# Performance work log

Measured on AMD Instinct MI355X. Metric: run time of the kernel, lower is better.

## Reference

```python
import jax, jax.numpy as jnp
import numpy as np

TAU = 0.95
COEF = 0.5
LOG_CLAMP = -100.0  # torch BCELoss clamps log terms at -100


def setup_inputs() -> dict:
    key = jax.random.key(0)
    k1, k2, k3, k4, k5 = jax.random.split(key, 5)
    B, L = 4096, 2048
    eps = 1e-4
    # probabilities in (eps, 1-eps) so log / log1p are finite
    def prob(k, shape):
        return jax.random.uniform(k, shape, dtype=jnp.float32, minval=eps, maxval=1.0 - eps)
    truncation_output = prob(k1, (B, L, 1))
    view_1_output = prob(k2, (B, L, 1))
    view_2_output = prob(k3, (B, L, 1))
    view_3_output = prob(k4, (B, L, 1))
    labels = (jax.random.uniform(k5, (B, L)) < 0.1).astype(jnp.float32)
    return {
        "truncation_output": truncation_output,
        "view_1_output": view_1_output,
        "view_2_output": view_2_output,
        "view_3_output": view_3_output,
        "labels": labels,
    }


def _bce_div_batch(p, y):
    # nn.BCELoss() (mean reduction) then .div(batch_size)
    logp = jnp.maximum(jnp.log(p), LOG_CLAMP)
    log1mp = jnp.maximum(jnp.log1p(-p), LOG_CLAMP)
    bce = -jnp.mean(y * logp + (1.0 - y) * log1mp)
    return bce / p.shape[0]


def _f1_matrix(labels):
    # r[i, j] = F1(labels[i], cutoff=j+1), vectorized via cumsum
    B, L = labels.shape
    cum = jnp.cumsum(labels, axis=1)                       # rel@(j+1)
    k = jnp.arange(1, L + 1, dtype=labels.dtype)           # cutoff
    total = cum[:, -1:]                                    # total relevant per row
    # P = cum/k, R = cum/total -> F1 = 2*cum/(k+total); 0 when no hits
    return jnp.where(cum > 0, 2.0 * cum / (k + total), 0.0)


def reference(truncation_output, view_1_output, view_2_output, view_3_output, labels):
    B = truncation_output.shape[0]
    v1 = _bce_div_batch(view_1_output[..., 0], labels)
    v2 = _bce_div_batch(view_2_output[..., 0], labels)
    v3 = _bce_div_batch(view_3_output[..., 0], labels)

    r = _f1_matrix(labels)                                 # [B, L]
    q = jax.nn.softmax(r / TAU, axis=-1)                   # softmax over list dim
    log_out = jnp.log(truncation_output[..., 0] / TAU)
    trunc_loss = -jnp.sum(log_out * q) / B

    return COEF * trunc_loss + (1.0 - COEF) * (v1 + v2 + v3)
```

## Files before the change

### kernel.cpp

```cpp
#include <hip/hip_runtime.h>

#define B_DIM 4096
#define L_DIM 2048
#define TPB   256
#define EPT   8
#define TAU_INV 1.0526315789473684f

__global__ __launch_bounds__(TPB) void milecut_row_kernel(
    const float* __restrict__ trunc,
    const float* __restrict__ view1,
    const float* __restrict__ view2,
    const float* __restrict__ view3,
    const float* __restrict__ labels,
    float* __restrict__ partials)
{
    const int row = blockIdx.x;
    const int t   = threadIdx.x;
    const size_t rowOff = (size_t)row * L_DIM;

    __shared__ float sdata[TPB];

    const float4* y4 = (const float4*)(labels + rowOff) + t * 2;
    float4 ya = y4[0];
    float4 yb = y4[1];
    float y[EPT] = {ya.x, ya.y, ya.z, ya.w, yb.x, yb.y, yb.z, yb.w};

    float lsum = 0.f;
    #pragma unroll
    for (int k = 0; k < EPT; ++k) lsum += y[k];

    sdata[t] = lsum;
    __syncthreads();
    for (int off = 1; off < TPB; off <<= 1) {
        float v   = sdata[t];
        float add = (t >= off) ? sdata[t - off] : 0.f;
        __syncthreads();
        sdata[t] = v + add;
        __syncthreads();
    }
    float total = sdata[TPB - 1];
    float run   = (t > 0) ? sdata[t - 1] : 0.f;
    __syncthreads();

    float x[EPT];
    float m = 0.f;
    #pragma unroll
    for (int k = 0; k < EPT; ++k) {
        run += y[k];
        float denom = (float)(t * EPT + k + 1) + total;
        float r = (run > 0.f) ? (2.f * run) / denom : 0.f;
        x[k] = r * TAU_INV;
        m = fmaxf(m, x[k]);
    }

    sdata[t] = m;
    __syncthreads();
    for (int off = TPB / 2; off > 0; off >>= 1) {
        if (t < off) sdata[t] = fmaxf(sdata[t], sdata[t + off]);
        __syncthreads();
    }
    m = sdata[0];
    __syncthreads();

    float esum = 0.f;
    #pragma unroll
    for (int k = 0; k < EPT; ++k) { x[k] = __expf(x[k] - m); esum += x[k]; }

    sdata[t] = esum;
    __syncthreads();
    for (int off = TPB / 2; off > 0; off >>= 1) {
        if (t < off) sdata[t] += sdata[t + off];
        __syncthreads();
    }
    float s = sdata[0];
    __syncthreads();

    const float4* t4 = (const float4*)(trunc + rowOff) + t * 2;
    float4 ta = t4[0];
    float4 tb = t4[1];
    float tv[EPT] = {ta.x, ta.y, ta.z, ta.w, tb.x, tb.y, tb.z, tb.w};
    float wtr = 0.f;
    #pragma unroll
    for (int k = 0; k < EPT; ++k) wtr += __logf(tv[k] * TAU_INV) * x[k];

    float bce = 0.f;
    const float* views[3] = {view1, view2, view3};
    #pragma unroll
    for (int vi = 0; vi < 3; ++vi) {
        const float4* p4 = (const float4*)(views[vi] + rowOff) + t * 2;
        float4 pa = p4[0];
        float4 pb = p4[1];
        float pv[EPT] = {pa.x, pa.y, pa.z, pa.w, pb.x, pb.y, pb.z, pb.w};
        #pragma unroll
        for (int k = 0; k < EPT; ++k) {
            float sel = (y[k] > 0.5f) ? pv[k] : (1.0f - pv[k]);
            bce += fmaxf(__logf(sel), -100.0f);
        }
    }

    sdata[t] = wtr;
    __syncthreads();
    for (int off = TPB / 2; off > 0; off >>= 1) {
        if (t < off) sdata[t] += sdata[t + off];
        __syncthreads();
    }
    float wsum = sdata[0];
    __syncthreads();

    sdata[t] = bce;
    __syncthreads();
    for (int off = TPB / 2; off > 0; off >>= 1) {
        if (t < off) sdata[t] += sdata[t + off];
        __syncthreads();
    }

    if (t == 0) {
        partials[row]         = wsum / s;
        partials[B_DIM + row] = sdata[0];
    }
}

__global__ __launch_bounds__(TPB) void milecut_final_kernel(
    const float* __restrict__ partials, float* __restrict__ out)
{
    const int t = threadIdx.x;
    float st = 0.f, sb = 0.f;
    for (int i = t; i < B_DIM; i += TPB) {
        st += partials[i];
        sb += partials[B_DIM + i];
    }
    __shared__ float s1[TPB];
    __shared__ float s2[TPB];
    s1[t] = st; s2[t] = sb;
    __syncthreads();
    for (int off = TPB / 2; off > 0; off >>= 1) {
        if (t < off) { s1[t] += s1[t + off]; s2[t] += s2[t + off]; }
        __syncthreads();
    }
    if (t == 0) {
        double St = (double)s1[0];
        double Sb = (double)s2[0];
        double trunc_loss = -St / (double)B_DIM;
        double vsum = -Sb / ((double)B_DIM * (double)L_DIM * (double)B_DIM);
        out[0] = (float)(0.5 * trunc_loss + 0.5 * vsum);
    }
}

extern "C" void kernel_launch(void* const* d_in, const int* in_sizes, int n_in,
                              void* d_out, int out_size, void* d_ws, size_t ws_size,
                              hipStream_t stream) {
    const float* trunc  = (const float*)d_in[0];
    const float* v1     = (const float*)d_in[1];
    const float* v2     = (const float*)d_in[2];
    const float* v3     = (const float*)d_in[3];
    const float* labels = (const float*)d_in[4];

    float* partials = (float*)d_ws;

    milecut_row_kernel<<<B_DIM, TPB, 0, stream>>>(trunc, v1, v2, v3, labels, partials);
    milecut_final_kernel<<<1, TPB, 0, stream>>>(partials, (float*)d_out);
}
```

Measured before the change: 180.3 us.

## Replace shared-memory block reductions with wavefront shuffles and hoist all loads

Replaces the shared-memory Hillis-Steele scan and tree reductions, which use many __syncthreads, with wavefront shuffle scans and reductions that need only two block barriers. All five input rows are loaded up front so their memory latency overlaps. The softmax max-subtraction pass is dropped because the F1 values lie in [0,1], so exp without the shift stays bounded; this removes one reduction. The gain is fewer barriers and less LDS traffic, at the cost of higher register pressure from holding all inputs at once.

```diff
diff --git a/kernel.cpp b/kernel.cpp
--- a/kernel.cpp
+++ b/kernel.cpp
@@ -4,6 +4,7 @@
 #define L_DIM 2048
 #define TPB   256
 #define EPT   8
+#define NWAVE (TPB / 64)
 #define TAU_INV 1.0526315789473684f
 
 __global__ __launch_bounds__(TPB) void milecut_row_kernel(
@@ -14,109 +15,98 @@
     const float* __restrict__ labels,
     float* __restrict__ partials)
 {
-    const int row = blockIdx.x;
-    const int t   = threadIdx.x;
+    const int row  = blockIdx.x;
+    const int t    = threadIdx.x;
+    const int lane = t & 63;
+    const int wave = t >> 6;
     const size_t rowOff = (size_t)row * L_DIM;
 
-    __shared__ float sdata[TPB];
+    const float4* y4 = (const float4*)(labels + rowOff) + t * 2;
+    const float4* t4 = (const float4*)(trunc  + rowOff) + t * 2;
+    const float4* p1 = (const float4*)(view1  + rowOff) + t * 2;
+    const float4* p2 = (const float4*)(view2  + rowOff) + t * 2;
+    const float4* p3 = (const float4*)(view3  + rowOff) + t * 2;
+    float4 ya = y4[0], yb = y4[1];
+    float4 ta = t4[0], tb = t4[1];
+    float4 v1a = p1[0], v1b = p1[1];
+    float4 v2a = p2[0], v2b = p2[1];
+    float4 v3a = p3[0], v3b = p3[1];
 
-    const float4* y4 = (const float4*)(labels + rowOff) + t * 2;
-    float4 ya = y4[0];
-    float4 yb = y4[1];
-    float y[EPT] = {ya.x, ya.y, ya.z, ya.w, yb.x, yb.y, yb.z, yb.w};
+    float y[EPT]  = {ya.x, ya.y, ya.z, ya.w, yb.x, yb.y, yb.z, yb.w};
 
     float lsum = 0.f;
     #pragma unroll
     for (int k = 0; k < EPT; ++k) lsum += y[k];
 
-    sdata[t] = lsum;
+    float v = lsum;
+    #pragma unroll
+    for (int off = 1; off < 64; off <<= 1) {
+        float n = __shfl_up(v, off, 64);
+        if (lane >= off) v += n;
+    }
+    float waveTotal = __shfl(v, 63, 64);
+
+    __shared__ float wtot[NWAVE];
+    __shared__ float red[NWAVE][3];
+    if (lane == 63) wtot[wave] = waveTotal;
     __syncthreads();
-    for (int off = 1; off < TPB; off <<= 1) {
-        float v   = sdata[t];
-        float add = (t >= off) ? sdata[t - off] : 0.f;
-        __syncthreads();
-        sdata[t] = v + add;
-        __syncthreads();
+    float wavePrefix = 0.f, total = 0.f;
+    #pragma unroll
+    for (int w = 0; w < NWAVE; ++w) {
+        float wt = wtot[w];
+        if (w < wave) wavePrefix += wt;
+        total += wt;
     }
-    float total = sdata[TPB - 1];
-    float run   = (t > 0) ? sdata[t - 1] : 0.f;
-    __syncthreads();
+    float run = wavePrefix + (v - lsum);
 
     float x[EPT];
-    float m = 0.f;
+    float esum = 0.f;
     #pragma unroll
     for (int k = 0; k < EPT; ++k) {
         run += y[k];
         float denom = (float)(t * EPT + k + 1) + total;
         float r = (run > 0.f) ? (2.f * run) / denom : 0.f;
-        x[k] = r * TAU_INV;
-        m = fmaxf(m, x[k]);
+        x[k] = __expf(r * TAU_INV);
+        esum += x[k];
     }
 
-    sdata[t] = m;
-    __syncthreads();
-    for (int off = TPB / 2; off > 0; off >>= 1) {
-        if (t < off) sdata[t] = fmaxf(sdata[t], sdata[t + off]);
-        __syncthreads();
-    }
-    m = sdata[0];
-    __syncthreads();
-
-    float esum = 0.f;
-    #pragma unroll
-    for (int k = 0; k < EPT; ++k) { x[k] = __expf(x[k] - m); esum += x[k]; }
-
-    sdata[t] = esum;
-    __syncthreads();
-    for (int off = TPB / 2; off > 0; off >>= 1) {
-        if (t < off) sdata[t] += sdata[t + off];
-        __syncthreads();
-    }
-    float s = sdata[0];
-    __syncthreads();
-
-    const float4* t4 = (const float4*)(trunc + rowOff) + t * 2;
-    float4 ta = t4[0];
-    float4 tb = t4[1];
     float tv[EPT] = {ta.x, ta.y, ta.z, ta.w, tb.x, tb.y, tb.z, tb.w};
     float wtr = 0.f;
     #pragma unroll
     for (int k = 0; k < EPT; ++k) wtr += __logf(tv[k] * TAU_INV) * x[k];
 
+    float pv1[EPT] = {v1a.x, v1a.y, v1a.z, v1a.w, v1b.x, v1b.y, v1b.z, v1b.w};
+    float pv2[EPT] = {v2a.x, v2a.y, v2a.z, v2a.w, v2b.x, v2b.y, v2b.z, v2b.w};
+    float pv3[EPT] = {v3a.x, v3a.y, v3a.z, v3a.w, v3b.x, v3b.y, v3b.z, v3b.w};
     float bce = 0.f;
-    const float* views[3] = {view1, view2, view3};
     #pragma unroll
-    for (int vi = 0; vi < 3; ++vi) {
-        const float4* p4 = (const float4*)(views[vi] + rowOff) + t * 2;
-        float4 pa = p4[0];
-        float4 pb = p4[1];
-        float pv[EPT] = {pa.x, pa.y, pa.z, pa.w, pb.x, pb.y, pb.z, pb.w};
-        #pragma unroll
-        for (int k = 0; k < EPT; ++k) {
-            float sel = (y[k] > 0.5f) ? pv[k] : (1.0f - pv[k]);
-            bce += fmaxf(__logf(sel), -100.0f);
-        }
+    for (int k = 0; k < EPT; ++k) {
+        bool pos = (y[k] > 0.5f);
+        float s1 = pos ? pv1[k] : (1.0f - pv1[k]);
+        float s2 = pos ? pv2[k] : (1.0f - pv2[k]);
+        float s3 = pos ? pv3[k] : (1.0f - pv3[k]);
+        bce += fmaxf(__logf(s1), -100.0f);
+        bce += fmaxf(__logf(s2), -100.0f);
+        bce += fmaxf(__logf(s3), -100.0f);
     }
 
-    sdata[t] = wtr;
-    __syncthreads();
-    for (int off = TPB / 2; off > 0; off >>= 1) {
-        if (t < off) sdata[t] += sdata[t + off];
-        __syncthreads();
+    #pragma unroll
+    for (int off = 32; off > 0; off >>= 1) {
+        esum += __shfl_down(esum, off, 64);
+        wtr  += __shfl_down(wtr,  off, 64);
+        bce  += __shfl_down(bce,  off, 64);
     }
-    float wsum = sdata[0];
+    if (lane == 0) { red[wave][0] = esum; red[wave][1] = wtr; red[wave][2] = bce; }
     __syncthreads();
 
-    sdata[t] = bce;
-    __syncthreads();
-    for (int off = TPB / 2; off > 0; off >>= 1) {
-        if (t < off) sdata[t] += sdata[t + off];
-        __syncthreads();
-    }
-
     if (t == 0) {
-        partials[row]         = wsum / s;
-        partials[B_DIM + row] = sdata[0];
+        float es = 0.f, wt = 0.f, bc = 0.f;
+        #pragma unroll
+        for (int w = 0; w < NWAVE; ++w) {
+            es += red[w][0]; wt += red[w][1]; bc += red[w][2];
+        }
+        partials[row]         = wt / es;
+        partials[B_DIM + row] = bc;
     }
 }
 
@@ -129,17 +119,20 @@
         st += partials[i];
         sb += partials[B_DIM + i];
     }
-    __shared__ float s1[TPB];
-    __shared__ float s2[TPB];
-    s1[t] = st; s2[t] = sb;
+    #pragma unroll
+    for (int off = 32; off > 0; off >>= 1) {
+        st += __shfl_down(st, off, 64);
+        sb += __shfl_down(sb, off, 64);
+    }
+    __shared__ float s1[NWAVE];
+    __shared__ float s2[NWAVE];
+    const int lane = t & 63, wave = t >> 6;
+    if (lane == 0) { s1[wave] = st; s2[wave] = sb; }
     __syncthreads();
-    for (int off = TPB / 2; off > 0; off >>= 1) {
-        if (t < off) { s1[t] += s1[t + off]; s2[t] += s2[t + off]; }
-        __syncthreads();
-    }
     if (t == 0) {
-        double St = (double)s1[0];
-        double Sb = (double)s2[0];
+        double St = 0.0, Sb = 0.0;
+        #pragma unroll
+        for (int w = 0; w < NWAVE; ++w) { St += (double)s1[w]; Sb += (double)s2[w]; }
         double trunc_loss = -St / (double)B_DIM;
         double vsum = -Sb / ((double)B_DIM * (double)L_DIM * (double)B_DIM);
         out[0] = (float)(0.5 * trunc_loss + 0.5 * vsum);
```

Result: no change. 181.0 us (+0.4%).
